# Optimization experiments

Hardware: AMD Instinct MI355X
Metric: run time of the kernel (lower is better)

Reference implementation:

```python
import jax, jax.numpy as jnp
import numpy as np

NEG_INF = -1.0e9  # matches torch masked_fill_ value


def setup_inputs() -> dict:
    key = jax.random.key(0)
    kq, kk, kv, km = jax.random.split(key, 4)
    B, H, S, D = 4, 16, 2048, 64
    Q = jax.random.normal(kq, (B, H, S, D), dtype=jnp.float32)
    K = jax.random.normal(kk, (B, H, S, D), dtype=jnp.float32)
    V = jax.random.normal(kv, (B, H, S, D), dtype=jnp.float32)
    attn_mask = jax.random.randint(km, (B, 1, 1, S), 0, 2).astype(jnp.bool_)
    return {"Q": Q, "K": K, "V": V, "attn_mask": attn_mask}


def reference(Q, K, V, attn_mask):
    d_k = Q.shape[-1]
    scale = 1.0 / jnp.sqrt(jnp.asarray(d_k, dtype=Q.dtype))
    # scores: [B, H, Sq, Sk]
    scores = jnp.einsum('bhqd,bhkd->bhqk', Q, K) * scale
    scores = jnp.where(attn_mask, jnp.asarray(NEG_INF, dtype=scores.dtype), scores)
    attn = jax.nn.softmax(scores, axis=-1)
    context = jnp.einsum('bhqk,bhkd->bhqd', attn, V)
    return (context, attn)
```

## Files before the change

kernel.cpp:

```cpp
#include <hip/hip_runtime.h>
#include <stdint.h>

#define B_    4
#define H_    16
#define S_    2048
#define D_    64
#define SCALE_LOG2E 0.1803368801111244f

typedef __bf16 bf16x8 __attribute__((ext_vector_type(8)));
typedef float  f32x4  __attribute__((ext_vector_type(4)));

__global__ __launch_bounds__(256)
void prep_k(const float* __restrict__ K, __bf16* __restrict__ img) {
    int t    = blockIdx.x * 256 + threadIdx.x;
    int tile = t >> 9;
    int L    = (t & 511) << 4;
    int row  = L >> 7;
    int cb   = L & 127;
    int scb  = cb ^ ((row & 7) << 4);
    int bh = tile >> 5, kt = tile & 31;
    const float* src = K + (((size_t)bh * S_ + kt * 64 + row) * D_ + (scb >> 1));
    float4 a = *reinterpret_cast<const float4*>(src);
    float4 b = *reinterpret_cast<const float4*>(src + 4);
    bf16x8 w = { (__bf16)a.x,(__bf16)a.y,(__bf16)a.z,(__bf16)a.w,
                 (__bf16)b.x,(__bf16)b.y,(__bf16)b.z,(__bf16)b.w };
    *reinterpret_cast<bf16x8*>((char*)img + ((size_t)t << 4)) = w;
}

__global__ __launch_bounds__(256)
void prep_v(const float* __restrict__ V, __bf16* __restrict__ img) {
    __shared__ float Ls[64][65];
    const int tid = threadIdx.x;
    const int bh = blockIdx.x >> 5, st = blockIdx.x & 31;
    const float* Vp = V + ((size_t)bh * S_ + st * 64) * D_;
    for (int i = tid; i < 1024; i += 256) {
        int r = i >> 4, c = (i & 15) << 2;
        float4 v = reinterpret_cast<const float4*>(Vp)[i];
        Ls[r][c] = v.x; Ls[r][c+1] = v.y; Ls[r][c+2] = v.z; Ls[r][c+3] = v.w;
    }
    __syncthreads();
    const int d = tid >> 2, sc = (tid & 3) * 16;
    bf16x8 w0, w1;
    #pragma unroll
    for (int j = 0; j < 8; ++j) w0[j] = (__bf16)Ls[sc + j][d];
    #pragma unroll
    for (int j = 0; j < 8; ++j) w1[j] = (__bf16)Ls[sc + 8 + j][d];
    char* tb = (char*)img + (size_t)(bh * 32 + st) * 8192;
    int sw = (d & 7) << 4;
    *reinterpret_cast<bf16x8*>(tb + d * 128 + ((sc * 2) ^ sw))      = w0;
    *reinterpret_cast<bf16x8*>(tb + d * 128 + ((sc * 2 + 16) ^ sw)) = w1;
}

__device__ __forceinline__ void gload16(const void* g, void* l) {
    __builtin_amdgcn_global_load_lds(
        (const __attribute__((address_space(1))) void*)g,
        (__attribute__((address_space(3))) void*)l, 16, 0, 0);
}

__global__ __launch_bounds__(256, 3)
void sdpa_main(const float* __restrict__ Q, const __bf16* __restrict__ Kimg,
               const __bf16* __restrict__ Vimg, const int* __restrict__ mask,
               float* __restrict__ ctx_out, float* __restrict__ attn_out)
{
    __shared__ __align__(16) __bf16 Kb[2][4096];
    __shared__ __align__(16) __bf16 Vb[2][4096];
    __shared__ __align__(16) float  Ps[4][16][68];

    const int tid = threadIdx.x;
    const int lane = tid & 63, wid = tid >> 6;
    const int l15 = lane & 15, lhi = lane >> 4;

    const int orig = blockIdx.x, cpx = gridDim.x >> 3;
    const int bid = (orig & 7) * cpx + (orig >> 3);
    const int qt = bid & 31, bh = bid >> 5, b = bh >> 4;

    const char* KimgT = (const char*)Kimg + (size_t)bh * 32 * 8192;
    const char* VimgT = (const char*)Vimg + (size_t)bh * 32 * 8192;
    const int*  mp = mask + b * S_;

    float* msc = &Ps[0][0][0];
    for (int i = tid; i < S_; i += 256) msc[i] = mp[i] ? 1.f : 0.f;

    {
        const char* src = KimgT + qt * 8192 + wid * 2048 + lane * 16;
        char* dst = (char*)&Kb[0][0] + wid * 2048;
        gload16(src,        dst);
        gload16(src + 1024, dst + 1024);
    }

    bf16x8 aQ0, aQ1;
    {
        const float* qrow = Q + ((size_t)bh * S_ + qt * 64 + wid * 16 + l15) * D_ + lhi * 8;
        float4 a = *reinterpret_cast<const float4*>(qrow);
        float4 c = *reinterpret_cast<const float4*>(qrow + 4);
        bf16x8 w0 = { (__bf16)a.x,(__bf16)a.y,(__bf16)a.z,(__bf16)a.w,
                      (__bf16)c.x,(__bf16)c.y,(__bf16)c.z,(__bf16)c.w };
        aQ0 = w0;
        a = *reinterpret_cast<const float4*>(qrow + 32);
        c = *reinterpret_cast<const float4*>(qrow + 36);
        bf16x8 w1 = { (__bf16)a.x,(__bf16)a.y,(__bf16)a.z,(__bf16)a.w,
                      (__bf16)c.x,(__bf16)c.y,(__bf16)c.z,(__bf16)c.w };
        aQ1 = w1;
    }

    __syncthreads();

    uint32_t m0 = 0, m1 = 0, m2 = 0, m3 = 0;
    #pragma unroll
    for (int kk = 0; kk < 8; ++kk) {
        #pragma unroll
        for (int sub = 0; sub < 4; ++sub) {
            int bit = kk * 4 + sub;
            if (msc[(kk     ) * 64 + sub * 16 + l15] != 0.f) m0 |= 1u << bit;
            if (msc[(kk +  8) * 64 + sub * 16 + l15] != 0.f) m1 |= 1u << bit;
            if (msc[(kk + 16) * 64 + sub * 16 + l15] != 0.f) m2 |= 1u << bit;
            if (msc[(kk + 24) * 64 + sub * 16 + l15] != 0.f) m3 |= 1u << bit;
        }
    }

    int fo[4][2];
    #pragma unroll
    for (int sub = 0; sub < 4; ++sub) {
        int row = sub * 16 + l15;
        int sw = (row & 7) << 4;
        fo[sub][0] = row * 128 + ((lhi * 16) ^ sw);
        fo[sub][1] = row * 128 + ((64 + lhi * 16) ^ sw);
    }

    float ls[4] = {0.f, 0.f, 0.f, 0.f};
    int cur = 0;
    for (int kt = 0; kt < 32; ++kt) {
        int e  = (kt + qt) & 31;
        int en = (kt + 1 + qt) & 31;
        {
            const char* src = KimgT + en * 8192 + wid * 2048 + lane * 16;
            char* dst = (char*)&Kb[cur ^ 1][0] + wid * 2048;
            gload16(src, dst); gload16(src + 1024, dst + 1024);
        }
        const char* kb = (const char*)&Kb[cur][0];
        uint32_t mw = (e & 16) ? ((e & 8) ? m3 : m2) : ((e & 8) ? m1 : m0);
        int mbase = (e & 7) * 4;
        #pragma unroll
        for (int sub = 0; sub < 4; ++sub) {
            bf16x8 b0 = *reinterpret_cast<const bf16x8*>(kb + fo[sub][0]);
            bf16x8 b1 = *reinterpret_cast<const bf16x8*>(kb + fo[sub][1]);
            f32x4 acc = {0.f, 0.f, 0.f, 0.f};
            acc = __builtin_amdgcn_mfma_f32_16x16x32_bf16(aQ0, b0, acc, 0, 0, 0);
            acc = __builtin_amdgcn_mfma_f32_16x16x32_bf16(aQ1, b1, acc, 0, 0, 0);
            float flag = ((mw >> (mbase + sub)) & 1) ? 0.f : 1.f;
            #pragma unroll
            for (int r = 0; r < 4; ++r)
                ls[r] += flag * exp2f(acc[r] * SCALE_LOG2E);
        }
        asm volatile("s_waitcnt vmcnt(0)" ::: "memory");
        __builtin_amdgcn_s_barrier();
        cur ^= 1;
    }
    float rl[4];
    #pragma unroll
    for (int r = 0; r < 4; ++r) {
        ls[r] += __shfl_xor(ls[r], 1);
        ls[r] += __shfl_xor(ls[r], 2);
        ls[r] += __shfl_xor(ls[r], 4);
        ls[r] += __shfl_xor(ls[r], 8);
        rl[r] = 1.0f / ls[r];
    }

    {
        const char* src = VimgT + qt * 8192 + wid * 2048 + lane * 16;
        char* dst = (char*)&Vb[cur][0] + wid * 2048;
        gload16(src, dst); gload16(src + 1024, dst + 1024);
    }
    asm volatile("s_waitcnt vmcnt(0)" ::: "memory");
    __builtin_amdgcn_s_barrier();

    f32x4 ctx[4];
    #pragma unroll
    for (int d = 0; d < 4; ++d) ctx[d] = (f32x4){0.f, 0.f, 0.f, 0.f};
    const size_t arow0 = (size_t)bh * S_ + (size_t)qt * 64 + wid * 16;

    for (int kt = 0; kt < 32; ++kt) {
        int e  = (kt + qt) & 31;
        int en = (kt + 1 + qt) & 31;
        {
            const char* ks = KimgT + en * 8192 + wid * 2048 + lane * 16;
            const char* vs = VimgT + en * 8192 + wid * 2048 + lane * 16;
            char* kd = (char*)&Kb[cur ^ 1][0] + wid * 2048;
            char* vd = (char*)&Vb[cur ^ 1][0] + wid * 2048;
            gload16(ks, kd); gload16(ks + 1024, kd + 1024);
            gload16(vs, vd); gload16(vs + 1024, vd + 1024);
        }
        const char* kb = (const char*)&Kb[cur][0];
        const char* vb = (const char*)&Vb[cur][0];
        uint32_t mw = (e & 16) ? ((e & 8) ? m3 : m2) : ((e & 8) ? m1 : m0);
        int mbase = (e & 7) * 4;

        #pragma unroll
        for (int sub = 0; sub < 4; ++sub) {
            bf16x8 b0 = *reinterpret_cast<const bf16x8*>(kb + fo[sub][0]);
            bf16x8 b1 = *reinterpret_cast<const bf16x8*>(kb + fo[sub][1]);
            f32x4 acc = {0.f, 0.f, 0.f, 0.f};
            acc = __builtin_amdgcn_mfma_f32_16x16x32_bf16(aQ0, b0, acc, 0, 0, 0);
            acc = __builtin_amdgcn_mfma_f32_16x16x32_bf16(aQ1, b1, acc, 0, 0, 0);
            float flag = ((mw >> (mbase + sub)) & 1) ? 0.f : 1.f;
            #pragma unroll
            for (int r = 0; r < 4; ++r) {
                float p = flag * exp2f(acc[r] * SCALE_LOG2E) * rl[r];
                Ps[wid][lhi * 4 + r][sub * 16 + l15] = p;
            }
        }

        #pragma unroll
        for (int it = 0; it < 4; ++it) {
            int idx = (it << 6) + lane;
            int r = idx >> 4, c = (idx & 15) << 2;
            float4 v = *reinterpret_cast<float4*>(&Ps[wid][r][c]);
            *reinterpret_cast<float4*>(&attn_out[(arow0 + r) * S_ + e * 64 + c]) = v;
        }

        bf16x8 aP0, aP1;
        {
            const float* s0 = &Ps[wid][l15][lhi * 8];
            f32x4 lo = *reinterpret_cast<const f32x4*>(s0);
            f32x4 hi = *reinterpret_cast<const f32x4*>(s0 + 4);
            bf16x8 t;
            t[0]=(__bf16)lo[0]; t[1]=(__bf16)lo[1]; t[2]=(__bf16)lo[2]; t[3]=(__bf16)lo[3];
            t[4]=(__bf16)hi[0]; t[5]=(__bf16)hi[1]; t[6]=(__bf16)hi[2]; t[7]=(__bf16)hi[3];
            aP0 = t;
            const float* s1 = &Ps[wid][l15][32 + lhi * 8];
            lo = *reinterpret_cast<const f32x4*>(s1);
            hi = *reinterpret_cast<const f32x4*>(s1 + 4);
            t[0]=(__bf16)lo[0]; t[1]=(__bf16)lo[1]; t[2]=(__bf16)lo[2]; t[3]=(__bf16)lo[3];
            t[4]=(__bf16)hi[0]; t[5]=(__bf16)hi[1]; t[6]=(__bf16)hi[2]; t[7]=(__bf16)hi[3];
            aP1 = t;
        }

        #pragma unroll
        for (int db = 0; db < 4; ++db) {
            bf16x8 v0 = *reinterpret_cast<const bf16x8*>(vb + fo[db][0]);
            bf16x8 v1 = *reinterpret_cast<const bf16x8*>(vb + fo[db][1]);
            ctx[db] = __builtin_amdgcn_mfma_f32_16x16x32_bf16(aP0, v0, ctx[db], 0, 0, 0);
            ctx[db] = __builtin_amdgcn_mfma_f32_16x16x32_bf16(aP1, v1, ctx[db], 0, 0, 0);
        }

        asm volatile("s_waitcnt vmcnt(0)" ::: "memory");
        __builtin_amdgcn_s_barrier();
        cur ^= 1;
    }

    #pragma unroll
    for (int db = 0; db < 4; ++db) {
        #pragma unroll
        for (int r = 0; r < 4; ++r) {
            ctx_out[(arow0 + lhi * 4 + r) * D_ + db * 16 + l15] = ctx[db][r];
        }
    }
}

extern "C" void kernel_launch(void* const* d_in, const int* in_sizes, int n_in,
                              void* d_out, int out_size, void* d_ws, size_t ws_size,
                              hipStream_t stream) {
    const float* Q    = (const float*)d_in[0];
    const float* K    = (const float*)d_in[1];
    const float* V    = (const float*)d_in[2];
    const int*   mask = (const int*)d_in[3];

    float* ctx_out  = (float*)d_out;
    float* attn_out = ctx_out + (size_t)B_ * H_ * S_ * D_;

    __bf16* Kimg = (__bf16*)d_ws;
    __bf16* Vimg = Kimg + (size_t)B_ * H_ * S_ * D_;

    prep_k<<<4096, 256, 0, stream>>>(K, Kimg);
    prep_v<<<B_ * H_ * 32, 256, 0, stream>>>(V, Vimg);
    sdpa_main<<<B_ * H_ * 32, 256, 0, stream>>>(Q, Kimg, Vimg, mask, ctx_out, attn_out);
}
```

Baseline: 405.6 us.

## Split key columns across waves with per-wave triple-buffered staging and cross-wave reduction

Each wave now owns a 16-key slice of every key tile and computes scores for all 64 query rows (Q kept in registers for four row blocks). This removes the block-wide barriers per tile and the shared-memory P round trip. K/V images are re-laid out per wave slice and staged with a private triple buffer, so waves advance independently. P is packed straight from MFMA outputs into the PV operand, and attn is stored directly as float4. The cost is a cross-wave reduction of row sums and of the context accumulators through shared memory, plus higher register pressure from 16 context accumulators.

Measured after the change: 727.5 us. 79.4% more time.

```diff
diff --git a/kernel.cpp b/kernel.cpp
--- a/kernel.cpp
+++ b/kernel.cpp
@@ -8,47 +8,51 @@
 #define SCALE_LOG2E 0.1803368801111244f
 
 typedef __bf16 bf16x8 __attribute__((ext_vector_type(8)));
+typedef __bf16 bf16x4 __attribute__((ext_vector_type(4)));
 typedef float  f32x4  __attribute__((ext_vector_type(4)));
 
 __global__ __launch_bounds__(256)
 void prep_k(const float* __restrict__ K, __bf16* __restrict__ img) {
-    int t    = blockIdx.x * 256 + threadIdx.x;
-    int tile = t >> 9;
-    int L    = (t & 511) << 4;
-    int row  = L >> 7;
-    int cb   = L & 127;
-    int scb  = cb ^ ((row & 7) << 4);
-    int bh = tile >> 5, kt = tile & 31;
-    const float* src = K + (((size_t)bh * S_ + kt * 64 + row) * D_ + (scb >> 1));
+    int t     = blockIdx.x * 256 + threadIdx.x;
+    int slice = t >> 7;
+    int L     = (t & 127) << 4;
+    int kp    = L >> 7;
+    int cb    = L & 127;
+    int scb   = cb ^ ((kp & 7) << 4);
+    int w  = slice & 3;
+    int e  = (slice >> 2) & 31;
+    int bh = slice >> 7;
+    int s  = e * 64 + w * 16 + kp;
+    const float* src = K + ((size_t)bh * S_ + s) * D_ + (scb >> 1);
     float4 a = *reinterpret_cast<const float4*>(src);
     float4 b = *reinterpret_cast<const float4*>(src + 4);
-    bf16x8 w = { (__bf16)a.x,(__bf16)a.y,(__bf16)a.z,(__bf16)a.w,
-                 (__bf16)b.x,(__bf16)b.y,(__bf16)b.z,(__bf16)b.w };
-    *reinterpret_cast<bf16x8*>((char*)img + ((size_t)t << 4)) = w;
+    bf16x8 wv = { (__bf16)a.x,(__bf16)a.y,(__bf16)a.z,(__bf16)a.w,
+                  (__bf16)b.x,(__bf16)b.y,(__bf16)b.z,(__bf16)b.w };
+    *reinterpret_cast<bf16x8*>((char*)img + ((size_t)t << 4)) = wv;
 }
 
 __global__ __launch_bounds__(256)
 void prep_v(const float* __restrict__ V, __bf16* __restrict__ img) {
     __shared__ float Ls[64][65];
     const int tid = threadIdx.x;
-    const int bh = blockIdx.x >> 5, st = blockIdx.x & 31;
-    const float* Vp = V + ((size_t)bh * S_ + st * 64) * D_;
+    const int bh = blockIdx.x >> 5, e = blockIdx.x & 31;
+    const float* Vp = V + ((size_t)bh * S_ + e * 64) * D_;
     for (int i = tid; i < 1024; i += 256) {
         int r = i >> 4, c = (i & 15) << 2;
         float4 v = reinterpret_cast<const float4*>(Vp)[i];
         Ls[r][c] = v.x; Ls[r][c+1] = v.y; Ls[r][c+2] = v.z; Ls[r][c+3] = v.w;
     }
     __syncthreads();
-    const int d = tid >> 2, sc = (tid & 3) * 16;
-    bf16x8 w0, w1;
-    #pragma unroll
-    for (int j = 0; j < 8; ++j) w0[j] = (__bf16)Ls[sc + j][d];
-    #pragma unroll
-    for (int j = 0; j < 8; ++j) w1[j] = (__bf16)Ls[sc + 8 + j][d];
-    char* tb = (char*)img + (size_t)(bh * 32 + st) * 8192;
-    int sw = (d & 7) << 4;
-    *reinterpret_cast<bf16x8*>(tb + d * 128 + ((sc * 2) ^ sw))      = w0;
-    *reinterpret_cast<bf16x8*>(tb + d * 128 + ((sc * 2 + 16) ^ sw)) = w1;
+    char* base = (char*)img + ((size_t)(bh * 32 + e) * 4) * 2048;
+    #pragma unroll
+    for (int m = tid; m < 512; m += 256) {
+        int d = m >> 3, w = (m >> 1) & 3, half = m & 1;
+        bf16x8 wv;
+        #pragma unroll
+        for (int j = 0; j < 8; ++j)
+            wv[j] = (__bf16)Ls[w * 16 + half * 8 + j][d];
+        *reinterpret_cast<bf16x8*>(base + (size_t)w * 2048 + d * 32 + half * 16) = wv;
+    }
 }
 
 __device__ __forceinline__ void gload16(const void* g, void* l) {
@@ -62,198 +66,193 @@
                const __bf16* __restrict__ Vimg, const int* __restrict__ mask,
                float* __restrict__ ctx_out, float* __restrict__ attn_out)
 {
-    __shared__ __align__(16) __bf16 Kb[2][4096];
-    __shared__ __align__(16) __bf16 Vb[2][4096];
-    __shared__ __align__(16) float  Ps[4][16][68];
+    __shared__ __align__(16) char smem[50176];
 
     const int tid = threadIdx.x;
     const int lane = tid & 63, wid = tid >> 6;
     const int l15 = lane & 15, lhi = lane >> 4;
+    const int sw = (l15 & 7) << 4;
 
     const int orig = blockIdx.x, cpx = gridDim.x >> 3;
     const int bid = (orig & 7) * cpx + (orig >> 3);
     const int qt = bid & 31, bh = bid >> 5, b = bh >> 4;
 
-    const char* KimgT = (const char*)Kimg + (size_t)bh * 32 * 8192;
-    const char* VimgT = (const char*)Vimg + (size_t)bh * 32 * 8192;
-    const int*  mp = mask + b * S_;
-
-    float* msc = &Ps[0][0][0];
-    for (int i = tid; i < S_; i += 256) msc[i] = mp[i] ? 1.f : 0.f;
-
-    {
-        const char* src = KimgT + qt * 8192 + wid * 2048 + lane * 16;
-        char* dst = (char*)&Kb[0][0] + wid * 2048;
-        gload16(src,        dst);
-        gload16(src + 1024, dst + 1024);
-    }
-
-    bf16x8 aQ0, aQ1;
-    {
-        const float* qrow = Q + ((size_t)bh * S_ + qt * 64 + wid * 16 + l15) * D_ + lhi * 8;
+    const char* kimg0 = (const char*)Kimg + (size_t)bh * 262144 + wid * 2048;
+    const char* vimg0 = (const char*)Vimg + (size_t)bh * 262144 + wid * 2048;
+    char* strip = smem + wid * 12288;
+
+    auto stageK = [&](int t) {
+        int e = (t + qt) & 31;
+        const char* s = kimg0 + (size_t)e * 8192 + lane * 16;
+        char* d = strip + (t % 3) * 4096;
+        gload16(s, d); gload16(s + 1024, d + 1024);
+    };
+    auto stageV = [&](int t) {
+        int e = (t + qt) & 31;
+        const char* s = vimg0 + (size_t)e * 8192 + lane * 16;
+        char* d = strip + (t % 3) * 4096 + 2048;
+        gload16(s, d); gload16(s + 1024, d + 1024);
+    };
+
+    bf16x8 bQ[4][2];
+    #pragma unroll
+    for (int rb = 0; rb < 4; ++rb) {
+        const float* qrow = Q + ((size_t)bh * S_ + qt * 64 + rb * 16 + l15) * D_ + lhi * 8;
         float4 a = *reinterpret_cast<const float4*>(qrow);
         float4 c = *reinterpret_cast<const float4*>(qrow + 4);
         bf16x8 w0 = { (__bf16)a.x,(__bf16)a.y,(__bf16)a.z,(__bf16)a.w,
                       (__bf16)c.x,(__bf16)c.y,(__bf16)c.z,(__bf16)c.w };
-        aQ0 = w0;
+        bQ[rb][0] = w0;
         a = *reinterpret_cast<const float4*>(qrow + 32);
         c = *reinterpret_cast<const float4*>(qrow + 36);
         bf16x8 w1 = { (__bf16)a.x,(__bf16)a.y,(__bf16)a.z,(__bf16)a.w,
                       (__bf16)c.x,(__bf16)c.y,(__bf16)c.z,(__bf16)c.w };
-        aQ1 = w1;
-    }
-
+        bQ[rb][1] = w1;
+    }
+
+    uint32_t mw[4] = {0, 0, 0, 0};
+    {
+        const int* mrow = mask + b * S_ + wid * 16 + lhi * 4;
+        #pragma unroll
+        for (int e = 0; e < 32; ++e) {
+            int4 mm = *reinterpret_cast<const int4*>(mrow + e * 64);
+            uint32_t nib = (mm.x ? 1u : 0u) | (mm.y ? 2u : 0u) |
+                           (mm.z ? 4u : 0u) | (mm.w ? 8u : 0u);
+            mw[e >> 3] |= nib << ((e & 7) * 4);
+        }
+    }
+
+    float ls[4] = {0.f, 0.f, 0.f, 0.f};
+    stageK(0);
+    for (int t = 0; t < 32; ++t) {
+        if (t < 31) {
+            stageK(t + 1);
+            asm volatile("s_waitcnt vmcnt(2)" ::: "memory");
+        } else {
+            asm volatile("s_waitcnt vmcnt(0)" ::: "memory");
+        }
+        const char* kb = strip + (t % 3) * 4096;
+        bf16x8 kf0 = *reinterpret_cast<const bf16x8*>(kb + l15 * 128 + ((lhi * 16) ^ sw));
+        bf16x8 kf1 = *reinterpret_cast<const bf16x8*>(kb + l15 * 128 + ((64 + lhi * 16) ^ sw));
+        int e = (t + qt) & 31;
+        uint32_t nib = (mw[e >> 3] >> ((e & 7) * 4)) & 15u;
+        #pragma unroll
+        for (int rb = 0; rb < 4; ++rb) {
+            f32x4 acc = {0.f, 0.f, 0.f, 0.f};
+            acc = __builtin_amdgcn_mfma_f32_16x16x32_bf16(kf0, bQ[rb][0], acc, 0, 0, 0);
+            acc = __builtin_amdgcn_mfma_f32_16x16x32_bf16(kf1, bQ[rb][1], acc, 0, 0, 0);
+            float p0 = (nib & 1u) ? 0.f : exp2f(acc[0] * SCALE_LOG2E);
+            float p1 = (nib & 2u) ? 0.f : exp2f(acc[1] * SCALE_LOG2E);
+            float p2 = (nib & 4u) ? 0.f : exp2f(acc[2] * SCALE_LOG2E);
+            float p3 = (nib & 8u) ? 0.f : exp2f(acc[3] * SCALE_LOG2E);
+            ls[rb] += (p0 + p1) + (p2 + p3);
+        }
+    }
+
+    #pragma unroll
+    for (int rb = 0; rb < 4; ++rb) {
+        ls[rb] += __shfl_xor(ls[rb], 16);
+        ls[rb] += __shfl_xor(ls[rb], 32);
+    }
+    float* lsb = reinterpret_cast<float*>(smem + 49152);
+    if (lhi == 0) {
+        #pragma unroll
+        for (int rb = 0; rb < 4; ++rb) lsb[(wid * 4 + rb) * 16 + l15] = ls[rb];
+    }
     __syncthreads();
-
-    uint32_t m0 = 0, m1 = 0, m2 = 0, m3 = 0;
-    #pragma unroll
-    for (int kk = 0; kk < 8; ++kk) {
-        #pragma unroll
-        for (int sub = 0; sub < 4; ++sub) {
-            int bit = kk * 4 + sub;
-            if (msc[(kk     ) * 64 + sub * 16 + l15] != 0.f) m0 |= 1u << bit;
-            if (msc[(kk +  8) * 64 + sub * 16 + l15] != 0.f) m1 |= 1u << bit;
-            if (msc[(kk + 16) * 64 + sub * 16 + l15] != 0.f) m2 |= 1u << bit;
-            if (msc[(kk + 24) * 64 + sub * 16 + l15] != 0.f) m3 |= 1u << bit;
-        }
-    }
-
-    int fo[4][2];
-    #pragma unroll
-    for (int sub = 0; sub < 4; ++sub) {
-        int row = sub * 16 + l15;
-        int sw = (row & 7) << 4;
-        fo[sub][0] = row * 128 + ((lhi * 16) ^ sw);
-        fo[sub][1] = row * 128 + ((64 + lhi * 16) ^ sw);
-    }
-
-    float ls[4] = {0.f, 0.f, 0.f, 0.f};
-    int cur = 0;
-    for (int kt = 0; kt < 32; ++kt) {
-        int e  = (kt + qt) & 31;
-        int en = (kt + 1 + qt) & 31;
-        {
-            const char* src = KimgT + en * 8192 + wid * 2048 + lane * 16;
-            char* dst = (char*)&Kb[cur ^ 1][0] + wid * 2048;
-            gload16(src, dst); gload16(src + 1024, dst + 1024);
-        }
-        const char* kb = (const char*)&Kb[cur][0];
-        uint32_t mw = (e & 16) ? ((e & 8) ? m3 : m2) : ((e & 8) ? m1 : m0);
-        int mbase = (e & 7) * 4;
-        #pragma unroll
-        for (int sub = 0; sub < 4; ++sub) {
-            bf16x8 b0 = *reinterpret_cast<const bf16x8*>(kb + fo[sub][0]);
-            bf16x8 b1 = *reinterpret_cast<const bf16x8*>(kb + fo[sub][1]);
+    float rl[4];
+    #pragma unroll
+    for (int rb = 0; rb < 4; ++rb) {
+        float tot = (lsb[rb * 16 + l15] + lsb[(4 + rb) * 16 + l15]) +
+                    (lsb[(8 + rb) * 16 + l15] + lsb[(12 + rb) * 16 + l15]);
+        rl[rb] = 1.0f / tot;
+    }
+
+    f32x4 ctx[4][4];
+    #pragma unroll
+    for (int rb = 0; rb < 4; ++rb)
+        #pragma unroll
+        for (int db = 0; db < 4; ++db) ctx[rb][db] = (f32x4){0.f, 0.f, 0.f, 0.f};
+
+    const size_t arowq = (size_t)bh * S_ + (size_t)qt * 64;
+
+    auto qkexp = [&](int t, bf16x4* pk) {
+        const char* kb = strip + (t % 3) * 4096;
+        bf16x8 kf0 = *reinterpret_cast<const bf16x8*>(kb + l15 * 128 + ((lhi * 16) ^ sw));
+        bf16x8 kf1 = *reinterpret_cast<const bf16x8*>(kb + l15 * 128 + ((64 + lhi * 16) ^ sw));
+        int e = (t + qt) & 31;
+        uint32_t nib = (mw[e >> 3] >> ((e & 7) * 4)) & 15u;
+        size_t colbase = (size_t)e * 64 + wid * 16 + lhi * 4;
+        #pragma unroll
+        for (int rb = 0; rb < 4; ++rb) {
             f32x4 acc = {0.f, 0.f, 0.f, 0.f};
-            acc = __builtin_amdgcn_mfma_f32_16x16x32_bf16(aQ0, b0, acc, 0, 0, 0);
-            acc = __builtin_amdgcn_mfma_f32_16x16x32_bf16(aQ1, b1, acc, 0, 0, 0);
-            float flag = ((mw >> (mbase + sub)) & 1) ? 0.f : 1.f;
+            acc = __builtin_amdgcn_mfma_f32_16x16x32_bf16(kf0, bQ[rb][0], acc, 0, 0, 0);
+            acc = __builtin_amdgcn_mfma_f32_16x16x32_bf16(kf1, bQ[rb][1], acc, 0, 0, 0);
+            float p0 = (nib & 1u) ? 0.f : exp2f(acc[0] * SCALE_LOG2E) * rl[rb];
+            float p1 = (nib & 2u) ? 0.f : exp2f(acc[1] * SCALE_LOG2E) * rl[rb];
+            float p2 = (nib & 4u) ? 0.f : exp2f(acc[2] * SCALE_LOG2E) * rl[rb];
+            float p3 = (nib & 8u) ? 0.f : exp2f(acc[3] * SCALE_LOG2E) * rl[rb];
+            float4 st = { p0, p1, p2, p3 };
+            *reinterpret_cast<float4*>(&attn_out[(arowq + rb * 16 + l15) * S_ + colbase]) = st;
+            bf16x4 pkk = { (__bf16)p0, (__bf16)p1, (__bf16)p2, (__bf16)p3 };
+            pk[rb] = pkk;
+        }
+    };
+
+    stageK(0); stageV(0);
+    bf16x4 pkA[4], pkB[4];
+    for (int tp = 0; tp < 16; ++tp) {
+        int t0 = tp * 2, t1 = t0 + 1;
+        stageK(t1); stageV(t1);
+        asm volatile("s_waitcnt vmcnt(4)" ::: "memory");
+        qkexp(t0, pkA);
+        if (tp < 15) {
+            stageK(t1 + 1); stageV(t1 + 1);
+            asm volatile("s_waitcnt vmcnt(4)" ::: "memory");
+        } else {
+            asm volatile("s_waitcnt vmcnt(0)" ::: "memory");
+        }
+        qkexp(t1, pkB);
+        const char* vb0 = strip + (t0 % 3) * 4096 + 2048;
+        const char* vb1 = strip + (t1 % 3) * 4096 + 2048;
+        #pragma unroll
+        for (int db = 0; db < 4; ++db) {
+            int off = (db * 16 + l15) * 32 + lhi * 8;
+            bf16x4 v0 = *reinterpret_cast<const bf16x4*>(vb0 + off);
+            bf16x4 v1 = *reinterpret_cast<const bf16x4*>(vb1 + off);
+            bf16x8 Bv;
+            Bv[0]=v0[0]; Bv[1]=v0[1]; Bv[2]=v0[2]; Bv[3]=v0[3];
+            Bv[4]=v1[0]; Bv[5]=v1[1]; Bv[6]=v1[2]; Bv[7]=v1[3];
             #pragma unroll
-            for (int r = 0; r < 4; ++r)
-                ls[r] += flag * exp2f(acc[r] * SCALE_LOG2E);
-        }
-        asm volatile("s_waitcnt vmcnt(0)" ::: "memory");
-        __builtin_amdgcn_s_barrier();
-        cur ^= 1;
-    }
-    float rl[4];
-    #pragma unroll
-    for (int r = 0; r < 4; ++r) {
-        ls[r] += __shfl_xor(ls[r], 1);
-        ls[r] += __shfl_xor(ls[r], 2);
-        ls[r] += __shfl_xor(ls[r], 4);
-        ls[r] += __shfl_xor(ls[r], 8);
-        rl[r] = 1.0f / ls[r];
-    }
-
-    {
-        const char* src = VimgT + qt * 8192 + wid * 2048 + lane * 16;
-        char* dst = (char*)&Vb[cur][0] + wid * 2048;
-        gload16(src, dst); gload16(src + 1024, dst + 1024);
-    }
-    asm volatile("s_waitcnt vmcnt(0)" ::: "memory");
-    __builtin_amdgcn_s_barrier();
-
-    f32x4 ctx[4];
-    #pragma unroll
-    for (int d = 0; d < 4; ++d) ctx[d] = (f32x4){0.f, 0.f, 0.f, 0.f};
-    const size_t arow0 = (size_t)bh * S_ + (size_t)qt * 64 + wid * 16;
-
-    for (int kt = 0; kt < 32; ++kt) {
-        int e  = (kt + qt) & 31;
-        int en = (kt + 1 + qt) & 31;
-        {
-            const char* ks = KimgT + en * 8192 + wid * 2048 + lane * 16;
-            const char* vs = VimgT + en * 8192 + wid * 2048 + lane * 16;
-            char* kd = (char*)&Kb[cur ^ 1][0] + wid * 2048;
-            char* vd = (char*)&Vb[cur ^ 1][0] + wid * 2048;
-            gload16(ks, kd); gload16(ks + 1024, kd + 1024);
-            gload16(vs, vd); gload16(vs + 1024, vd + 1024);
-        }
-        const char* kb = (const char*)&Kb[cur][0];
-        const char* vb = (const char*)&Vb[cur][0];
-        uint32_t mw = (e & 16) ? ((e & 8) ? m3 : m2) : ((e & 8) ? m1 : m0);
-        int mbase = (e & 7) * 4;
-
-        #pragma unroll
-        for (int sub = 0; sub < 4; ++sub) {
-            bf16x8 b0 = *reinterpret_cast<const bf16x8*>(kb + fo[sub][0]);
-            bf16x8 b1 = *reinterpret_cast<const bf16x8*>(kb + fo[sub][1]);
-            f32x4 acc = {0.f, 0.f, 0.f, 0.f};
-            acc = __builtin_amdgcn_mfma_f32_16x16x32_bf16(aQ0, b0, acc, 0, 0, 0);
-            acc = __builtin_amdgcn_mfma_f32_16x16x32_bf16(aQ1, b1, acc, 0, 0, 0);
-            float flag = ((mw >> (mbase + sub)) & 1) ? 0.f : 1.f;
+            for (int rb = 0; rb < 4; ++rb) {
+                bf16x8 Av;
+                Av[0]=pkA[rb][0]; Av[1]=pkA[rb][1]; Av[2]=pkA[rb][2]; Av[3]=pkA[rb][3];
+                Av[4]=pkB[rb][0]; Av[5]=pkB[rb][1]; Av[6]=pkB[rb][2]; Av[7]=pkB[rb][3];
+                ctx[rb][db] = __builtin_amdgcn_mfma_f32_16x16x32_bf16(Av, Bv, ctx[rb][db], 0, 0, 0);
+            }
+        }
+    }
+
+    __syncthreads();
+    float* Cred = reinterpret_cast<float*>(smem);
+    for (int ph = 0; ph < 4; ++ph) {
+        if (wid == ph) {
             #pragma unroll
-            for (int r = 0; r < 4; ++r) {
-                float p = flag * exp2f(acc[r] * SCALE_LOG2E) * rl[r];
-                Ps[wid][lhi * 4 + r][sub * 16 + l15] = p;
-            }
-        }
-
-        #pragma unroll
-        for (int it = 0; it < 4; ++it) {
-            int idx = (it << 6) + lane;
-            int r = idx >> 4, c = (idx & 15) << 2;
-            float4 v = *reinterpret_cast<float4*>(&Ps[wid][r][c]);
-            *reinterpret_cast<float4*>(&attn_out[(arow0 + r) * S_ + e * 64 + c]) = v;
-        }
-
-        bf16x8 aP0, aP1;
-        {
-            const float* s0 = &Ps[wid][l15][lhi * 8];
-            f32x4 lo = *reinterpret_cast<const f32x4*>(s0);
-            f32x4 hi = *reinterpret_cast<const f32x4*>(s0 + 4);
-            bf16x8 t;
-            t[0]=(__bf16)lo[0]; t[1]=(__bf16)lo[1]; t[2]=(__bf16)lo[2]; t[3]=(__bf16)lo[3];
-            t[4]=(__bf16)hi[0]; t[5]=(__bf16)hi[1]; t[6]=(__bf16)hi[2]; t[7]=(__bf16)hi[3];
-            aP0 = t;
-            const float* s1 = &Ps[wid][l15][32 + lhi * 8];
-            lo = *reinterpret_cast<const f32x4*>(s1);
-            hi = *reinterpret_cast<const f32x4*>(s1 + 4);
-            t[0]=(__bf16)lo[0]; t[1]=(__bf16)lo[1]; t[2]=(__bf16)lo[2]; t[3]=(__bf16)lo[3];
-            t[4]=(__bf16)hi[0]; t[5]=(__bf16)hi[1]; t[6]=(__bf16)hi[2]; t[7]=(__bf16)hi[3];
-            aP1 = t;
-        }
-
-        #pragma unroll
-        for (int db = 0; db < 4; ++db) {
-            bf16x8 v0 = *reinterpret_cast<const bf16x8*>(vb + fo[db][0]);
-            bf16x8 v1 = *reinterpret_cast<const bf16x8*>(vb + fo[db][1]);
-            ctx[db] = __builtin_amdgcn_mfma_f32_16x16x32_bf16(aP0, v0, ctx[db], 0, 0, 0);
-            ctx[db] = __builtin_amdgcn_mfma_f32_16x16x32_bf16(aP1, v1, ctx[db], 0, 0, 0);
-        }
-
-        asm volatile("s_waitcnt vmcnt(0)" ::: "memory");
-        __builtin_amdgcn_s_barrier();
-        cur ^= 1;
-    }
-
-    #pragma unroll
-    for (int db = 0; db < 4; ++db) {
-        #pragma unroll
-        for (int r = 0; r < 4; ++r) {
-            ctx_out[(arow0 + lhi * 4 + r) * D_ + db * 16 + l15] = ctx[db][r];
-        }
+            for (int rb = 0; rb < 4; ++rb)
+                #pragma unroll
+                for (int db = 0; db < 4; ++db)
+                    #pragma unroll
+                    for (int r = 0; r < 4; ++r) {
+                        float* c = &Cred[(rb * 16 + lhi * 4 + r) * 65 + db * 16 + l15];
+                        if (ph == 0) *c = ctx[rb][db][r];
+                        else         *c += ctx[rb][db][r];
+                    }
+        }
+        __syncthreads();
+    }
+    for (int i = tid; i < 4096; i += 256) {
+        int q = i >> 6, d = i & 63;
+        ctx_out[(arowq + q) * D_ + d] = Cred[q * 65 + d];
     }
 }
 
```
